# Kernel tuning notes

Measured on AMD Instinct MI355X. Metric: run time of the kernel, lower is better.

Reference implementation:

```python
import jax, jax.numpy as jnp
import numpy as np

N = 4096       # nodes in the exchange pool
H = 256        # hidden_dim
L = 3          # num_layers (GATConv stack)
TIMESTEP = 350
TOTAL = 700
EDGE_P = 0.01  # adjacency density


def setup_inputs() -> dict:
    key = jax.random.key(0)
    ks = jax.random.split(key, 12)
    s = 0.05
    adj = (jax.random.uniform(ks[0], (N, N)) < EDGE_P).astype(jnp.float32)
    arrival = jax.random.uniform(ks[1], (N,)) * 300.0
    departure = arrival + 1.0 + jax.random.uniform(ks[2], (N,)) * 300.0
    hard = (jax.random.uniform(ks[3], (N,)) < 0.3).astype(jnp.float32)
    mask = jax.random.bernoulli(ks[4], 0.7, (N,))
    return dict(
        adj_matrix=adj, arrival=arrival, departure=departure,
        is_hard_to_match=hard, mask=mask,
        emb_W1=jax.random.normal(ks[5], (2, H)) * s,
        emb_b1=jnp.zeros((H,)),
        emb_W2=jax.random.normal(ks[6], (H, H)) * s,
        emb_b2=jnp.zeros((H,)),
        gat_W=jax.random.normal(ks[7], (L, H, H)) * s,
        gat_asrc=jax.random.normal(ks[8], (L, H)) * s,
        gat_adst=jax.random.normal(ks[9], (L, H)) * s,
        gat_bias=jnp.zeros((L, H)),
        sel_W=jax.random.normal(ks[10], (H + 1, 1)) * s,
        sel_b=jnp.zeros((1,)),
        timestep=TIMESTEP,
        total_timesteps=TOTAL,
    )


def reference(adj_matrix, arrival, departure, is_hard_to_match, mask,
              emb_W1, emb_b1, emb_W2, emb_b2,
              gat_W, gat_asrc, gat_adst, gat_bias,
              sel_W, sel_b, timestep, total_timesteps):
    n = adj_matrix.shape[0]
    # progress feature; denom guarded (inactive nodes are zeroed at the end anyway)
    denom = departure - arrival
    progress = (timestep - arrival) / jnp.where(denom != 0, denom, 1.0)
    in_data = jnp.stack([progress, is_hard_to_match], axis=1)      # [N,2]
    x = (in_data @ emb_W1 + emb_b1) @ emb_W2 + emb_b2               # [N,H] (two Linears, no act)

    # active-subgraph edges (adj[np.ix_(masked, masked)].nonzero()) + one self loop per node
    em = (adj_matrix != 0) & mask[:, None] & mask[None, :]
    em = em.at[jnp.arange(n), jnp.arange(n)].set(True)              # GATConv add_self_loops

    h = x
    for l in range(L):
        hw = h @ gat_W[l]                                           # [N,H]
        a_s = hw @ gat_asrc[l]                                      # [N] per-source score
        a_d = hw @ gat_adst[l]                                      # [N] per-dest score
        e = jax.nn.leaky_relu(a_s[:, None] + a_d[None, :], 0.2)     # e[i,j]: src i -> dst j
        alpha = jax.nn.softmax(jnp.where(em, e, -1e9), axis=0)      # softmax over incoming srcs
        h = alpha.T @ hw + gat_bias[l]                              # out[j] = sum_i alpha[i,j] hw[i]
        if l < L - 1:
            h = jax.nn.relu(h)                                      # BasicGNN act between layers

    x = x + h                                                       # residual
    mu = jnp.mean(x, axis=-1, keepdims=True)                        # F.layer_norm, no affine
    var = jnp.mean((x - mu) ** 2, axis=-1, keepdims=True)
    x = (x - mu) * jax.lax.rsqrt(var + 1e-5)

    tctx = jnp.full((n, 1), timestep / total_timesteps, x.dtype)
    logits = jnp.concatenate([x, tctx], axis=1) @ sel_W + sel_b
    out = jax.nn.sigmoid(logits)                                    # [N,1]
    return jnp.where(mask[:, None], out, 0.0)                       # scatter into zeros
```

## Files before the change

kernel.cpp:

```cpp
#include <hip/hip_runtime.h>
#include <math.h>

#define N 4096
#define H 256
#define LAYERS 3
#define CAP 128
#define NPB 16

__device__ __forceinline__ float block_reduce_sum(float v, float* sm) {
    int tid = threadIdx.x;
    sm[tid] = v;
    __syncthreads();
    for (int s = 128; s > 0; s >>= 1) {
        if (tid < s) sm[tid] += sm[tid + s];
        __syncthreads();
    }
    float r = sm[0];
    __syncthreads();
    return r;
}

__global__ void k_init_edges(int* __restrict__ cnt, int* __restrict__ edges) {
    int j = blockIdx.x * blockDim.x + threadIdx.x;
    if (j < N) {
        cnt[j] = 1;
        edges[j * CAP] = j;
    }
}

__global__ void k_build_edges(const float* __restrict__ adj, const int* __restrict__ mask,
                              int* __restrict__ cnt, int* __restrict__ edges) {
    int i = blockIdx.x;
    if (!mask[i]) return;
    const float* row = adj + (size_t)i * N;
    for (int j = threadIdx.x; j < N; j += blockDim.x) {
        if (j != i && row[j] != 0.0f && mask[j]) {
            int slot = atomicAdd(&cnt[j], 1);
            if (slot < CAP) edges[j * CAP + slot] = i;
        }
    }
}

__global__ void k_embed(const float* __restrict__ arrival, const float* __restrict__ departure,
                        const float* __restrict__ hard,
                        const float* __restrict__ W1, const float* __restrict__ b1,
                        const float* __restrict__ W2, const float* __restrict__ b2,
                        const int* __restrict__ t_ts,
                        float* __restrict__ x) {
    __shared__ float t_lds[NPB][H];
    int tid = threadIdx.x;
    int base = blockIdx.x * NPB;
    float ts = (float)t_ts[0];
    for (int idx = tid; idx < NPB * H; idx += 256) {
        int p = idx >> 8, hh = idx & (H - 1);
        int n = base + p;
        float den = departure[n] - arrival[n];
        if (den == 0.f) den = 1.f;
        float prog = (ts - arrival[n]) / den;
        t_lds[p][hh] = prog * W1[hh] + hard[n] * W1[H + hh] + b1[hh];
    }
    __syncthreads();
    float acc[NPB];
#pragma unroll
    for (int p = 0; p < NPB; ++p) acc[p] = 0.f;
    for (int hh = 0; hh < H; ++hh) {
        float w = W2[hh * H + tid];
#pragma unroll
        for (int p = 0; p < NPB; ++p) acc[p] += t_lds[p][hh] * w;
    }
#pragma unroll
    for (int p = 0; p < NPB; ++p)
        x[(size_t)(base + p) * H + tid] = acc[p] + b2[tid];
}

__global__ void k_matmul(const float* __restrict__ hin, const float* __restrict__ W,
                         float* __restrict__ hw) {
    __shared__ float t_lds[NPB][H];
    int tid = threadIdx.x;
    int base = blockIdx.x * NPB;
    for (int idx = tid; idx < NPB * H; idx += 256) {
        int p = idx >> 8, hh = idx & (H - 1);
        t_lds[p][hh] = hin[(size_t)(base + p) * H + hh];
    }
    __syncthreads();
    float acc[NPB];
#pragma unroll
    for (int p = 0; p < NPB; ++p) acc[p] = 0.f;
    for (int hh = 0; hh < H; ++hh) {
        float w = W[hh * H + tid];
#pragma unroll
        for (int p = 0; p < NPB; ++p) acc[p] += t_lds[p][hh] * w;
    }
#pragma unroll
    for (int p = 0; p < NPB; ++p)
        hw[(size_t)(base + p) * H + tid] = acc[p];
}

__global__ void k_scores(const float* __restrict__ hw, const float* __restrict__ asrc,
                         const float* __restrict__ adst,
                         float* __restrict__ a_s, float* __restrict__ a_d) {
    __shared__ float sm[256];
    int n = blockIdx.x, tid = threadIdx.x;
    float v = hw[(size_t)n * H + tid];
    float s1 = block_reduce_sum(v * asrc[tid], sm);
    float s2 = block_reduce_sum(v * adst[tid], sm);
    if (tid == 0) { a_s[n] = s1; a_d[n] = s2; }
}

__global__ void k_aggregate(const float* __restrict__ hw, const float* __restrict__ a_s,
                            const float* __restrict__ a_d, const int* __restrict__ cnt,
                            const int* __restrict__ edges, const float* __restrict__ bias,
                            float* __restrict__ hout, int do_relu) {
    __shared__ float red[256];
    __shared__ float w_lds[CAP];
    __shared__ int   i_lds[CAP];
    int j = blockIdx.x, tid = threadIdx.x;
    int c = cnt[j];
    if (c > CAP) c = CAP;
    float e = -INFINITY;
    if (tid < c) {
        int i = edges[j * CAP + tid];
        i_lds[tid] = i;
        float v = a_s[i] + a_d[j];
        e = (v > 0.f) ? v : 0.2f * v;
    }
    red[tid] = e;
    __syncthreads();
    for (int s = 128; s > 0; s >>= 1) {
        if (tid < s) red[tid] = fmaxf(red[tid], red[tid + s]);
        __syncthreads();
    }
    float m = red[0];
    __syncthreads();
    float w = 0.f;
    if (tid < c) { w = __expf(e - m); w_lds[tid] = w; }
    red[tid] = w;
    __syncthreads();
    for (int s = 128; s > 0; s >>= 1) {
        if (tid < s) red[tid] += red[tid + s];
        __syncthreads();
    }
    float inv = 1.f / red[0];
    __syncthreads();
    float acc = 0.f;
    for (int k = 0; k < c; ++k)
        acc += w_lds[k] * hw[(size_t)i_lds[k] * H + tid];
    float o = acc * inv + bias[tid];
    if (do_relu) o = fmaxf(o, 0.f);
    hout[(size_t)j * H + tid] = o;
}

__global__ void k_final(const float* __restrict__ x, const float* __restrict__ h,
                        const int* __restrict__ mask,
                        const float* __restrict__ selW, const float* __restrict__ selb,
                        const int* __restrict__ t_ts, const int* __restrict__ t_tot,
                        float* __restrict__ out) {
    __shared__ float sm[256];
    int n = blockIdx.x, tid = threadIdx.x;
    float v = x[(size_t)n * H + tid] + h[(size_t)n * H + tid];
    float mean = block_reduce_sum(v, sm) * (1.f / H);
    float d = v - mean;
    float var = block_reduce_sum(d * d, sm) * (1.f / H);
    float xn = d * rsqrtf(var + 1e-5f);
    float dot = block_reduce_sum(xn * selW[tid], sm);
    if (tid == 0) {
        float tctx = (float)t_ts[0] / (float)t_tot[0];
        float logit = dot + tctx * selW[H] + selb[0];
        float s = 1.f / (1.f + __expf(-logit));
        out[n] = mask[n] ? s : 0.f;
    }
}

extern "C" void kernel_launch(void* const* d_in, const int* in_sizes, int n_in,
                              void* d_out, int out_size, void* d_ws, size_t ws_size,
                              hipStream_t stream) {
    const float* adj       = (const float*)d_in[0];
    const float* arrival   = (const float*)d_in[1];
    const float* departure = (const float*)d_in[2];
    const float* hard      = (const float*)d_in[3];
    const int*   mask      = (const int*)d_in[4];
    const float* embW1     = (const float*)d_in[5];
    const float* embb1     = (const float*)d_in[6];
    const float* embW2     = (const float*)d_in[7];
    const float* embb2     = (const float*)d_in[8];
    const float* gatW      = (const float*)d_in[9];
    const float* gatasrc   = (const float*)d_in[10];
    const float* gatadst   = (const float*)d_in[11];
    const float* gatbias   = (const float*)d_in[12];
    const float* selW      = (const float*)d_in[13];
    const float* selb      = (const float*)d_in[14];
    const int*   ts        = (const int*)d_in[15];
    const int*   tot       = (const int*)d_in[16];
    float* out = (float*)d_out;

    float* ws  = (float*)d_ws;
    float* x   = ws;
    float* h   = x  + (size_t)N * H;
    float* hw  = h  + (size_t)N * H;
    float* a_s = hw + (size_t)N * H;
    float* a_d = a_s + N;
    int*   cnt   = (int*)(a_d + N);
    int*   edges = cnt + N;

    k_init_edges<<<N / 256, 256, 0, stream>>>(cnt, edges);
    k_build_edges<<<N, 256, 0, stream>>>(adj, mask, cnt, edges);
    k_embed<<<N / NPB, 256, 0, stream>>>(arrival, departure, hard,
                                         embW1, embb1, embW2, embb2, ts, x);
    for (int l = 0; l < LAYERS; ++l) {
        const float* hin = (l == 0) ? x : h;
        k_matmul<<<N / NPB, 256, 0, stream>>>(hin, gatW + (size_t)l * H * H, hw);
        k_scores<<<N, 256, 0, stream>>>(hw, gatasrc + l * H, gatadst + l * H, a_s, a_d);
        k_aggregate<<<N, 256, 0, stream>>>(hw, a_s, a_d, cnt, edges,
                                           gatbias + l * H, h, l < LAYERS - 1 ? 1 : 0);
    }
    k_final<<<N, 256, 0, stream>>>(x, h, mask, selW, selb, ts, tot, out);
}
```

Baseline: 206.9 us.

## Fuse score computation into matmul, final layernorm into aggregate, use wave-shuffle reductions

Attention score dot products are now computed inside the GAT matmul kernel, so the separate per-node scores launch is gone. The final residual, layernorm and sigmoid head run in the last aggregate kernel, removing the standalone final kernel. Tree reductions through shared memory are replaced with 64-lane wave shuffles. The edge build reads float4 with an early skip of all-zero quads, and the matmul LDS tile is transposed so each step reads float4. Together these cut launches, global traffic and barriers, at the cost of extra LDS reuse and syncs inside the matmul.

```diff
diff --git a/kernel.cpp b/kernel.cpp
--- a/kernel.cpp
+++ b/kernel.cpp
@@ -1,217 +1,222 @@
 #include <hip/hip_runtime.h>
-#include <math.h>
-
 #define N 4096
 #define H 256
-#define LAYERS 3
 #define CAP 128
 #define NPB 16
 
-__device__ __forceinline__ float block_reduce_sum(float v, float* sm) {
-    int tid = threadIdx.x;
-    sm[tid] = v;
-    __syncthreads();
-    for (int s = 128; s > 0; s >>= 1) {
-        if (tid < s) sm[tid] += sm[tid + s];
-        __syncthreads();
-    }
-    float r = sm[0];
+__device__ __forceinline__ float brs(float v, float* s4) {
+    int ln = threadIdx.x & 63, wv = threadIdx.x >> 6;
+#pragma unroll
+    for (int o = 32; o; o >>= 1) v += __shfl_xor(v, o, 64);
+    if (ln == 0) s4[wv] = v;
+    __syncthreads();
+    float r = s4[0] + s4[1] + s4[2] + s4[3];
     __syncthreads();
     return r;
 }
 
-__global__ void k_init_edges(int* __restrict__ cnt, int* __restrict__ edges) {
+__device__ __forceinline__ float brm(float v, float* s4) {
+    int ln = threadIdx.x & 63, wv = threadIdx.x >> 6;
+#pragma unroll
+    for (int o = 32; o; o >>= 1) v = fmaxf(v, __shfl_xor(v, o, 64));
+    if (ln == 0) s4[wv] = v;
+    __syncthreads();
+    float r = fmaxf(fmaxf(s4[0], s4[1]), fmaxf(s4[2], s4[3]));
+    __syncthreads();
+    return r;
+}
+
+__global__ void k_init(int* cnt, int* eg) {
     int j = blockIdx.x * blockDim.x + threadIdx.x;
-    if (j < N) {
-        cnt[j] = 1;
-        edges[j * CAP] = j;
-    }
-}
-
-__global__ void k_build_edges(const float* __restrict__ adj, const int* __restrict__ mask,
-                              int* __restrict__ cnt, int* __restrict__ edges) {
+    if (j < N) { cnt[j] = 1; eg[j * CAP] = j; }
+}
+
+__global__ void k_edges(const float* __restrict__ adj, const int* __restrict__ mask,
+                        int* cnt, int* eg) {
     int i = blockIdx.x;
     if (!mask[i]) return;
-    const float* row = adj + (size_t)i * N;
-    for (int j = threadIdx.x; j < N; j += blockDim.x) {
-        if (j != i && row[j] != 0.0f && mask[j]) {
-            int slot = atomicAdd(&cnt[j], 1);
-            if (slot < CAP) edges[j * CAP + slot] = i;
-        }
-    }
-}
-
-__global__ void k_embed(const float* __restrict__ arrival, const float* __restrict__ departure,
-                        const float* __restrict__ hard,
+    const float4* row = (const float4*)(adj + (size_t)i * N);
+    int tid = threadIdx.x;
+    for (int it = 0; it < 4; ++it) {
+        int j4 = it * 256 + tid;
+        float4 v = row[j4];
+        if (v.x == 0.f && v.y == 0.f && v.z == 0.f && v.w == 0.f) continue;
+        int j = j4 * 4;
+        if (v.x != 0.f && j     != i && mask[j    ]) { int s = atomicAdd(&cnt[j    ], 1); if (s < CAP) eg[(size_t)(j    ) * CAP + s] = i; }
+        if (v.y != 0.f && j + 1 != i && mask[j + 1]) { int s = atomicAdd(&cnt[j + 1], 1); if (s < CAP) eg[(size_t)(j + 1) * CAP + s] = i; }
+        if (v.z != 0.f && j + 2 != i && mask[j + 2]) { int s = atomicAdd(&cnt[j + 2], 1); if (s < CAP) eg[(size_t)(j + 2) * CAP + s] = i; }
+        if (v.w != 0.f && j + 3 != i && mask[j + 3]) { int s = atomicAdd(&cnt[j + 3], 1); if (s < CAP) eg[(size_t)(j + 3) * CAP + s] = i; }
+    }
+}
+
+__global__ void k_embed(const float* __restrict__ ar, const float* __restrict__ dp,
+                        const float* __restrict__ hd,
                         const float* __restrict__ W1, const float* __restrict__ b1,
                         const float* __restrict__ W2, const float* __restrict__ b2,
-                        const int* __restrict__ t_ts,
-                        float* __restrict__ x) {
-    __shared__ float t_lds[NPB][H];
-    int tid = threadIdx.x;
-    int base = blockIdx.x * NPB;
-    float ts = (float)t_ts[0];
+                        const int* __restrict__ tts, float* __restrict__ x) {
+    __shared__ float A[H * NPB];
+    int tid = threadIdx.x, base = blockIdx.x * NPB;
+    float ts = (float)tts[0];
+    for (int idx = tid; idx < NPB * H; idx += 256) {
+        int hh = idx >> 4, p = idx & (NPB - 1);
+        int n = base + p;
+        float den = dp[n] - ar[n];
+        if (den == 0.f) den = 1.f;
+        A[idx] = ((ts - ar[n]) / den) * W1[hh] + hd[n] * W1[H + hh] + b1[hh];
+    }
+    __syncthreads();
+    float acc[NPB];
+#pragma unroll
+    for (int p = 0; p < NPB; ++p) acc[p] = 0.f;
+    for (int hh = 0; hh < H; ++hh) {
+        float w = W2[(size_t)hh * H + tid];
+        const float4* t4 = (const float4*)(A + hh * NPB);
+#pragma unroll
+        for (int q = 0; q < 4; ++q) {
+            float4 a = t4[q];
+            acc[q*4+0] += a.x * w; acc[q*4+1] += a.y * w;
+            acc[q*4+2] += a.z * w; acc[q*4+3] += a.w * w;
+        }
+    }
+#pragma unroll
+    for (int p = 0; p < NPB; ++p)
+        x[(size_t)(base + p) * H + tid] = acc[p] + b2[tid];
+}
+
+__global__ void k_mm(const float* __restrict__ hin, const float* __restrict__ W,
+                     const float* __restrict__ as_, const float* __restrict__ ad_,
+                     float* __restrict__ hw, float* __restrict__ sa, float* __restrict__ sd) {
+    __shared__ float A[H * NPB];
+    int tid = threadIdx.x, base = blockIdx.x * NPB;
     for (int idx = tid; idx < NPB * H; idx += 256) {
         int p = idx >> 8, hh = idx & (H - 1);
-        int n = base + p;
-        float den = departure[n] - arrival[n];
-        if (den == 0.f) den = 1.f;
-        float prog = (ts - arrival[n]) / den;
-        t_lds[p][hh] = prog * W1[hh] + hard[n] * W1[H + hh] + b1[hh];
+        A[hh * NPB + p] = hin[(size_t)(base + p) * H + hh];
     }
     __syncthreads();
     float acc[NPB];
 #pragma unroll
     for (int p = 0; p < NPB; ++p) acc[p] = 0.f;
     for (int hh = 0; hh < H; ++hh) {
-        float w = W2[hh * H + tid];
-#pragma unroll
-        for (int p = 0; p < NPB; ++p) acc[p] += t_lds[p][hh] * w;
-    }
-#pragma unroll
-    for (int p = 0; p < NPB; ++p)
-        x[(size_t)(base + p) * H + tid] = acc[p] + b2[tid];
-}
-
-__global__ void k_matmul(const float* __restrict__ hin, const float* __restrict__ W,
-                         float* __restrict__ hw) {
-    __shared__ float t_lds[NPB][H];
-    int tid = threadIdx.x;
-    int base = blockIdx.x * NPB;
-    for (int idx = tid; idx < NPB * H; idx += 256) {
-        int p = idx >> 8, hh = idx & (H - 1);
-        t_lds[p][hh] = hin[(size_t)(base + p) * H + hh];
-    }
-    __syncthreads();
-    float acc[NPB];
-#pragma unroll
-    for (int p = 0; p < NPB; ++p) acc[p] = 0.f;
-    for (int hh = 0; hh < H; ++hh) {
-        float w = W[hh * H + tid];
-#pragma unroll
-        for (int p = 0; p < NPB; ++p) acc[p] += t_lds[p][hh] * w;
-    }
-#pragma unroll
-    for (int p = 0; p < NPB; ++p)
-        hw[(size_t)(base + p) * H + tid] = acc[p];
-}
-
-__global__ void k_scores(const float* __restrict__ hw, const float* __restrict__ asrc,
-                         const float* __restrict__ adst,
-                         float* __restrict__ a_s, float* __restrict__ a_d) {
-    __shared__ float sm[256];
-    int n = blockIdx.x, tid = threadIdx.x;
-    float v = hw[(size_t)n * H + tid];
-    float s1 = block_reduce_sum(v * asrc[tid], sm);
-    float s2 = block_reduce_sum(v * adst[tid], sm);
-    if (tid == 0) { a_s[n] = s1; a_d[n] = s2; }
-}
-
-__global__ void k_aggregate(const float* __restrict__ hw, const float* __restrict__ a_s,
-                            const float* __restrict__ a_d, const int* __restrict__ cnt,
-                            const int* __restrict__ edges, const float* __restrict__ bias,
-                            float* __restrict__ hout, int do_relu) {
-    __shared__ float red[256];
-    __shared__ float w_lds[CAP];
-    __shared__ int   i_lds[CAP];
+        float w = W[(size_t)hh * H + tid];
+        const float4* t4 = (const float4*)(A + hh * NPB);
+#pragma unroll
+        for (int q = 0; q < 4; ++q) {
+            float4 a = t4[q];
+            acc[q*4+0] += a.x * w; acc[q*4+1] += a.y * w;
+            acc[q*4+2] += a.z * w; acc[q*4+3] += a.w * w;
+        }
+    }
+#pragma unroll
+    for (int p = 0; p < NPB; ++p) hw[(size_t)(base + p) * H + tid] = acc[p];
+    __syncthreads();
+#pragma unroll
+    for (int p = 0; p < NPB; ++p) A[p * H + tid] = acc[p];
+    __syncthreads();
+    int wv = tid >> 6, ln = tid & 63;
+    for (int p = wv; p < NPB; p += 4) {
+        float v1 = 0.f, v2 = 0.f;
+#pragma unroll
+        for (int q = 0; q < 4; ++q) {
+            float t = A[p * H + ln + 64 * q];
+            v1 += t * as_[ln + 64 * q];
+            v2 += t * ad_[ln + 64 * q];
+        }
+#pragma unroll
+        for (int o = 32; o; o >>= 1) {
+            v1 += __shfl_xor(v1, o, 64);
+            v2 += __shfl_xor(v2, o, 64);
+        }
+        if (ln == 0) { sa[base + p] = v1; sd[base + p] = v2; }
+    }
+}
+
+__global__ void k_agg(const float* __restrict__ hw, const float* __restrict__ sa,
+                      const float* __restrict__ sd, const int* __restrict__ cnt,
+                      const int* __restrict__ eg, const float* __restrict__ bias,
+                      float* __restrict__ hout, int relu, int fin,
+                      const float* __restrict__ x, const int* __restrict__ mask,
+                      const float* __restrict__ sW, const float* __restrict__ sb,
+                      const int* __restrict__ tts, const int* __restrict__ ttot,
+                      float* __restrict__ out) {
+    __shared__ float s4[4];
+    __shared__ float wl[CAP];
+    __shared__ int il[CAP];
     int j = blockIdx.x, tid = threadIdx.x;
     int c = cnt[j];
     if (c > CAP) c = CAP;
     float e = -INFINITY;
     if (tid < c) {
-        int i = edges[j * CAP + tid];
-        i_lds[tid] = i;
-        float v = a_s[i] + a_d[j];
+        int i = eg[(size_t)j * CAP + tid];
+        il[tid] = i;
+        float v = sa[i] + sd[j];
         e = (v > 0.f) ? v : 0.2f * v;
     }
-    red[tid] = e;
-    __syncthreads();
-    for (int s = 128; s > 0; s >>= 1) {
-        if (tid < s) red[tid] = fmaxf(red[tid], red[tid + s]);
-        __syncthreads();
-    }
-    float m = red[0];
-    __syncthreads();
+    float m = brm(e, s4);
     float w = 0.f;
-    if (tid < c) { w = __expf(e - m); w_lds[tid] = w; }
-    red[tid] = w;
-    __syncthreads();
-    for (int s = 128; s > 0; s >>= 1) {
-        if (tid < s) red[tid] += red[tid + s];
-        __syncthreads();
-    }
-    float inv = 1.f / red[0];
+    if (tid < c) { w = __expf(e - m); wl[tid] = w; }
+    float inv = 1.f / brs(w, s4);
     __syncthreads();
     float acc = 0.f;
     for (int k = 0; k < c; ++k)
-        acc += w_lds[k] * hw[(size_t)i_lds[k] * H + tid];
+        acc += wl[k] * hw[(size_t)il[k] * H + tid];
     float o = acc * inv + bias[tid];
-    if (do_relu) o = fmaxf(o, 0.f);
-    hout[(size_t)j * H + tid] = o;
-}
-
-__global__ void k_final(const float* __restrict__ x, const float* __restrict__ h,
-                        const int* __restrict__ mask,
-                        const float* __restrict__ selW, const float* __restrict__ selb,
-                        const int* __restrict__ t_ts, const int* __restrict__ t_tot,
-                        float* __restrict__ out) {
-    __shared__ float sm[256];
-    int n = blockIdx.x, tid = threadIdx.x;
-    float v = x[(size_t)n * H + tid] + h[(size_t)n * H + tid];
-    float mean = block_reduce_sum(v, sm) * (1.f / H);
-    float d = v - mean;
-    float var = block_reduce_sum(d * d, sm) * (1.f / H);
-    float xn = d * rsqrtf(var + 1e-5f);
-    float dot = block_reduce_sum(xn * selW[tid], sm);
-    if (tid == 0) {
-        float tctx = (float)t_ts[0] / (float)t_tot[0];
-        float logit = dot + tctx * selW[H] + selb[0];
-        float s = 1.f / (1.f + __expf(-logit));
-        out[n] = mask[n] ? s : 0.f;
+    if (!fin) {
+        if (relu) o = fmaxf(o, 0.f);
+        hout[(size_t)j * H + tid] = o;
+    } else {
+        float v = x[(size_t)j * H + tid] + o;
+        float mn = brs(v, s4) * (1.f / H);
+        float d = v - mn;
+        float vr = brs(d * d, s4) * (1.f / H);
+        float xn = d * rsqrtf(vr + 1e-5f);
+        float dot = brs(xn * sW[tid], s4);
+        if (tid == 0) {
+            float lg = dot + ((float)tts[0] / (float)ttot[0]) * sW[H] + sb[0];
+            out[j] = mask[j] ? 1.f / (1.f + __expf(-lg)) : 0.f;
+        }
     }
 }
 
 extern "C" void kernel_launch(void* const* d_in, const int* in_sizes, int n_in,
                               void* d_out, int out_size, void* d_ws, size_t ws_size,
                               hipStream_t stream) {
-    const float* adj       = (const float*)d_in[0];
-    const float* arrival   = (const float*)d_in[1];
-    const float* departure = (const float*)d_in[2];
-    const float* hard      = (const float*)d_in[3];
-    const int*   mask      = (const int*)d_in[4];
-    const float* embW1     = (const float*)d_in[5];
-    const float* embb1     = (const float*)d_in[6];
-    const float* embW2     = (const float*)d_in[7];
-    const float* embb2     = (const float*)d_in[8];
-    const float* gatW      = (const float*)d_in[9];
-    const float* gatasrc   = (const float*)d_in[10];
-    const float* gatadst   = (const float*)d_in[11];
-    const float* gatbias   = (const float*)d_in[12];
-    const float* selW      = (const float*)d_in[13];
-    const float* selb      = (const float*)d_in[14];
-    const int*   ts        = (const int*)d_in[15];
-    const int*   tot       = (const int*)d_in[16];
+    const float* adj = (const float*)d_in[0];
+    const float* ar  = (const float*)d_in[1];
+    const float* dp  = (const float*)d_in[2];
+    const float* hd  = (const float*)d_in[3];
+    const int*   mk  = (const int*)d_in[4];
+    const float* eW1 = (const float*)d_in[5];
+    const float* eb1 = (const float*)d_in[6];
+    const float* eW2 = (const float*)d_in[7];
+    const float* eb2 = (const float*)d_in[8];
+    const float* gW  = (const float*)d_in[9];
+    const float* gas = (const float*)d_in[10];
+    const float* gad = (const float*)d_in[11];
+    const float* gb  = (const float*)d_in[12];
+    const float* sW  = (const float*)d_in[13];
+    const float* sb  = (const float*)d_in[14];
+    const int*   ts  = (const int*)d_in[15];
+    const int*   tt  = (const int*)d_in[16];
     float* out = (float*)d_out;
 
     float* ws  = (float*)d_ws;
     float* x   = ws;
     float* h   = x  + (size_t)N * H;
     float* hw  = h  + (size_t)N * H;
-    float* a_s = hw + (size_t)N * H;
-    float* a_d = a_s + N;
-    int*   cnt   = (int*)(a_d + N);
-    int*   edges = cnt + N;
-
-    k_init_edges<<<N / 256, 256, 0, stream>>>(cnt, edges);
-    k_build_edges<<<N, 256, 0, stream>>>(adj, mask, cnt, edges);
-    k_embed<<<N / NPB, 256, 0, stream>>>(arrival, departure, hard,
-                                         embW1, embb1, embW2, embb2, ts, x);
-    for (int l = 0; l < LAYERS; ++l) {
-        const float* hin = (l == 0) ? x : h;
-        k_matmul<<<N / NPB, 256, 0, stream>>>(hin, gatW + (size_t)l * H * H, hw);
-        k_scores<<<N, 256, 0, stream>>>(hw, gatasrc + l * H, gatadst + l * H, a_s, a_d);
-        k_aggregate<<<N, 256, 0, stream>>>(hw, a_s, a_d, cnt, edges,
-                                           gatbias + l * H, h, l < LAYERS - 1 ? 1 : 0);
-    }
-    k_final<<<N, 256, 0, stream>>>(x, h, mask, selW, selb, ts, tot, out);
-}
+    float* sa  = hw + (size_t)N * H;
+    float* sd  = sa + N;
+    int*   cnt = (int*)(sd + N);
+    int*   eg  = cnt + N;
+
+    k_init<<<N / 256, 256, 0, stream>>>(cnt, eg);
+    k_edges<<<N, 256, 0, stream>>>(adj, mk, cnt, eg);
+    k_embed<<<N / NPB, 256, 0, stream>>>(ar, dp, hd, eW1, eb1, eW2, eb2, ts, x);
+    for (int l = 0; l < 3; ++l) {
+        int last = (l == 2);
+        k_mm<<<N / NPB, 256, 0, stream>>>((l == 0) ? x : h, gW + (size_t)l * H * H,
+                                          gas + (size_t)l * H, gad + (size_t)l * H,
+                                          hw, sa, sd);
+        k_agg<<<N, 256, 0, stream>>>(hw, sa, sd, cnt, eg, gb + (size_t)l * H, h,
+                                     !last, last, x, mk, sW, sb, ts, tt, out);
+    }
+}
```

After: 189.8 us. 1.09x faster.
